# Optimization experiments

Measured on AMD Instinct MI355X. Metric: run time of the kernel, lower is better.

Reference implementation:

```python
import jax, jax.numpy as jnp
import numpy as np
from jax import lax

B, L, D, H, N, V, K = 2, 1024, 512, 8, 4, 32000, 64
HD = D // H


def layer_norm(x, g, b, eps=1e-5):
    m = jnp.mean(x, axis=-1, keepdims=True)
    v = jnp.var(x, axis=-1, keepdims=True)
    return (x - m) * lax.rsqrt(v + eps) * g + b


def setup_inputs() -> dict:
    ks = jax.random.split(jax.random.key(0), 16)
    s = 0.02
    return {
        "x_q": jax.random.normal(ks[0], (B, L, D), jnp.float32),
        "x": jax.random.randint(ks[1], (B, L), 0, V, jnp.int32),
        "E_slots": jax.random.normal(ks[2], (V, D), jnp.float32),
        "rhos": jax.random.uniform(ks[3], (N,), jnp.float32, 0.9, 0.999),
        "C_seq": jax.random.uniform(ks[4], (B, L, N), jnp.float32),
        "c_base": jax.random.uniform(ks[5], (B, K, N), jnp.float32),
        "unique_slots": jax.random.randint(ks[6], (B, K), 0, V, jnp.int32),
        "pad_mask": jnp.ones((B, K), jnp.bool_),
        "Wq": jax.random.normal(ks[7], (D, D), jnp.float32) * s,
        "Wk": jax.random.normal(ks[8], (D, D), jnp.float32) * s,
        "Wv": jax.random.normal(ks[9], (D, D), jnp.float32) * s,
        "Wo": jax.random.normal(ks[10], (D, D), jnp.float32) * s,
        "W_pe": jax.random.normal(ks[11], (N, D), jnp.float32) * s,
        "ln_kv_g": jnp.ones((D,), jnp.float32),
        "ln_kv_b": jnp.zeros((D,), jnp.float32),
        "ln_q_g": jnp.ones((D,), jnp.float32),
        "ln_q_b": jnp.zeros((D,), jnp.float32),
    }


def reference(x_q, x, E_slots, rhos, C_seq, c_base, unique_slots, pad_mask,
              Wq, Wk, Wv, Wo, W_pe, ln_kv_g, ln_kv_b, ln_q_g, ln_q_b):
    # --- projections (dropout is eval-mode identity) ---
    memory_base = layer_norm(E_slots, ln_kv_g, ln_kv_b)          # [V,D]
    E_k = (memory_base @ Wk).reshape(V, H, HD)                   # [V,H,hd]
    E_v = (memory_base @ Wv).reshape(V, H, HD)
    P_gate = (C_seq + 1.0) @ W_pe                                # [B,L,D]
    Q = layer_norm(x_q * P_gate, ln_q_g, ln_q_b) @ Wq            # [B,L,D]

    # --- initial EMA state from history ---
    safe = jnp.maximum(unique_slots, 0)                          # [B,K]
    ek0 = E_k[safe]                                              # [B,K,H,hd]
    ev0 = E_v[safe]
    outer0 = ek0[..., :, None] * ev0[..., None, :]               # [B,K,H,hd,hd]
    cb = c_base * pad_mask[..., None].astype(c_base.dtype)
    S0 = jnp.einsum('bkn,bkhij->bhnij', cb, outer0).astype(jnp.float32)  # [B,H,N,hd,hd]

    W_pe_hn = W_pe.reshape(N, H, HD).transpose(1, 0, 2)          # [H,N,hd]
    rhos_b = rhos[None, None, :, None, None]

    Qh = Q.reshape(B, L, H, HD).transpose(1, 0, 2, 3)            # [L,B,H,hd]
    toks = x.T                                                   # [L,B]

    def step(S, inp):
        q_t, tok = inp                                           # [B,H,hd], [B]
        S = S * rhos_b                                           # decay
        q_mod = q_t[:, :, None, :] * W_pe_hn[None]               # [B,H,N,hd]
        o_t = jnp.einsum('bhnd,bhnde->bhe', q_mod, S)            # sum over n, contract d
        ek_t = E_k[tok]                                          # [B,H,hd]
        ev_t = E_v[tok]
        outer = ek_t[..., :, None] * ev_t[..., None, :]          # [B,H,hd,hd]
        S = S + outer[:, :, None]                                # broadcast over N
        return S, o_t

    _, O = lax.scan(step, S0, (Qh, toks))                        # O: [L,B,H,hd]
    O = O.transpose(1, 0, 2, 3).reshape(B, L, D)
    return O @ Wo
```

## Files before the change

### kernel.cpp

```cpp
#include <hip/hip_runtime.h>
#include <stdint.h>

namespace {

constexpr int B = 2, L = 1024, D = 512, H = 8, N = 4, KSL = 64;
constexpr int CHK = 64;
constexpr int NCK = L / CHK;
constexpr int ROWS = B * L + B * KSL;

static_assert(D == 512 && N == 4, "layout assumptions");

typedef _Float16 half8 __attribute__((ext_vector_type(8)));
typedef _Float16 half4v __attribute__((ext_vector_type(4)));
typedef _Float16 half2t __attribute__((ext_vector_type(2)));
typedef float f32x4 __attribute__((ext_vector_type(4)));

__device__ __forceinline__ void gld16(_Float16* lds_dst, const _Float16* gsrc) {
  __builtin_amdgcn_global_load_lds(
      (const __attribute__((address_space(1))) unsigned int*)gsrc,
      (__attribute__((address_space(3))) unsigned int*)lds_dst, 16, 0, 0);
}

__global__ __launch_bounds__(256) void k_pre(
    const float* __restrict__ Wk, const float* __restrict__ Wv,
    const float* __restrict__ Wq, const float* __restrict__ Wo,
    _Float16* __restrict__ WTh,
    const float* __restrict__ E_slots, const int* __restrict__ x,
    const int* __restrict__ uniq, const float* __restrict__ kv_g,
    const float* __restrict__ kv_b, _Float16* __restrict__ lnEh,
    const float* __restrict__ x_q, const float* __restrict__ C_seq,
    const float* __restrict__ W_pe, const float* __restrict__ q_g,
    const float* __restrict__ q_b, _Float16* __restrict__ lnqh) {
  __shared__ _Float16 trh[64 * 66];
  __shared__ float red[8];
  int bid = blockIdx.x;
  int t = threadIdx.x;

  if (bid < 256) {
    int widx = bid >> 6, tile = bid & 63;
    int k0 = (tile >> 3) * 64, n0 = (tile & 7) * 64;
    const float* W = widx == 0 ? Wk : widx == 1 ? Wv : widx == 2 ? Wq : Wo;
#pragma unroll
    for (int i = 0; i < 16; ++i) {
      int idx = t + i * 256, r = idx >> 6, c = idx & 63;
      trh[c * 66 + r] = (_Float16)W[(size_t)(k0 + r) * 512 + n0 + c];
    }
    __syncthreads();
    _Float16* WT = WTh + (size_t)widx * 512 * 512;
#pragma unroll
    for (int i = 0; i < 8; ++i) {
      int idx = t + i * 256, rr = idx >> 5, cc = (idx & 31) * 2;
      half2t v = {trh[rr * 66 + cc], trh[rr * 66 + cc + 1]};
      *(half2t*)&WT[(size_t)(n0 + rr) * 512 + k0 + cc] = v;
    }
    return;
  }

  float vx, vy;
  const float* g;
  const float* bb;
  _Float16* dst;
  int d0 = t * 2;
  if (bid < 256 + ROWS) {
    int r = bid - 256;
    int idx;
    if (r < B * L) {
      idx = x[r];
    } else {
      int u = uniq[r - B * L];
      idx = u > 0 ? u : 0;
    }
    float2 v = *(const float2*)(E_slots + (size_t)idx * D + d0);
    vx = v.x;
    vy = v.y;
    g = kv_g; bb = kv_b;
    dst = lnEh + (size_t)r * D + d0;
  } else {
    int r = bid - 256 - ROWS;
    float c0 = C_seq[r * 4 + 0] + 1.f;
    float c1 = C_seq[r * 4 + 1] + 1.f;
    float c2 = C_seq[r * 4 + 2] + 1.f;
    float c3 = C_seq[r * 4 + 3] + 1.f;
    float p0 = c0 * W_pe[d0] + c1 * W_pe[512 + d0] + c2 * W_pe[1024 + d0] + c3 * W_pe[1536 + d0];
    float p1 = c0 * W_pe[d0 + 1] + c1 * W_pe[513 + d0] + c2 * W_pe[1025 + d0] + c3 * W_pe[1537 + d0];
    float2 xv = *(const float2*)(x_q + (size_t)r * D + d0);
    vx = xv.x * p0;
    vy = xv.y * p1;
    g = q_g; bb = q_b;
    dst = lnqh + (size_t)r * D + d0;
  }
  float s = vx + vy;
  float s2 = vx * vx + vy * vy;
#pragma unroll
  for (int o = 32; o > 0; o >>= 1) {
    s += __shfl_down(s, o);
    s2 += __shfl_down(s2, o);
  }
  if ((t & 63) == 0) {
    red[(t >> 6) * 2] = s;
    red[(t >> 6) * 2 + 1] = s2;
  }
  __syncthreads();
  float S = red[0] + red[2] + red[4] + red[6];
  float S2 = red[1] + red[3] + red[5] + red[7];
  float m = S * (1.f / D);
  float inv = rsqrtf(S2 * (1.f / D) - m * m + 1e-5f);
  half2t o2;
  o2.x = (_Float16)((vx - m) * inv * g[d0] + bb[d0]);
  o2.y = (_Float16)((vy - m) * inv * g[d0 + 1] + bb[d0 + 1]);
  *(half2t*)dst = o2;
}

__global__ __launch_bounds__(512) void k_gemm3(
    const _Float16* __restrict__ A0, const _Float16* __restrict__ Wt0, _Float16* __restrict__ C0, int M0,
    const _Float16* __restrict__ A1, const _Float16* __restrict__ Wt1, _Float16* __restrict__ C1, int M1,
    const _Float16* __restrict__ A2, const _Float16* __restrict__ Wt2, _Float16* __restrict__ C2, int M2) {
  const _Float16* A;
  const _Float16* Wt;
  _Float16* C;
  int M;
  int z = blockIdx.z;
  if (z == 0) { A = A0; Wt = Wt0; C = C0; M = M0; }
  else if (z == 1) { A = A1; Wt = Wt1; C = C1; M = M1; }
  else { A = A2; Wt = Wt2; C = C2; M = M2; }
  int m0 = blockIdx.y * 128;
  if (m0 >= M) return;
  int n0 = blockIdx.x * 128;

  __shared__ _Float16 As[2][128 * 64];
  __shared__ _Float16 Ws[2][128 * 64];

  int t = threadIdx.x;
  int lane = t & 63, w = t >> 6;
  int wr = (w >> 1) * 32, wc = (w & 1) * 64;
  int fr = lane & 15, kg = (lane >> 4) * 8;
  int kq = kg >> 3, fx = fr & 7;
  int pA = kq ^ fx, pB = (4 + kq) ^ fx;

  int srow = t >> 3;
  int sseg = ((t & 7) ^ (srow & 7)) * 8;
  int wbase = w * 512;

  const _Float16* gA = A + (size_t)(m0 + srow) * 512 + sseg;
  const _Float16* gB = Wt + (size_t)(n0 + srow) * 512 + sseg;

  f32x4 zero4 = {0.f, 0.f, 0.f, 0.f};
  f32x4 acc[2][4];
#pragma unroll
  for (int i = 0; i < 2; ++i)
#pragma unroll
    for (int j = 0; j < 4; ++j) acc[i][j] = zero4;

  gld16(&As[0][wbase], gA);
  gld16(&As[0][wbase + 4096], gA + 64 * 512);
  gld16(&Ws[0][wbase], gB);
  gld16(&Ws[0][wbase + 4096], gB + 64 * 512);
  __syncthreads();

  int buf = 0;
  for (int s8 = 0; s8 < 8; ++s8) {
    if (s8 < 7) {
      int k0 = (s8 + 1) * 64;
      gld16(&As[buf ^ 1][wbase], gA + k0);
      gld16(&As[buf ^ 1][wbase + 4096], gA + 64 * 512 + k0);
      gld16(&Ws[buf ^ 1][wbase], gB + k0);
      gld16(&Ws[buf ^ 1][wbase + 4096], gB + 64 * 512 + k0);
    }
    half8 af[2][2], bf[4][2];
#pragma unroll
    for (int mt = 0; mt < 2; ++mt) {
      int row = wr + mt * 16 + fr;
      af[mt][0] = *(const half8*)&As[buf][row * 64 + pA * 8];
      af[mt][1] = *(const half8*)&As[buf][row * 64 + pB * 8];
    }
#pragma unroll
    for (int nt = 0; nt < 4; ++nt) {
      int row = wc + nt * 16 + fr;
      bf[nt][0] = *(const half8*)&Ws[buf][row * 64 + pA * 8];
      bf[nt][1] = *(const half8*)&Ws[buf][row * 64 + pB * 8];
    }
#pragma unroll
    for (int mt = 0; mt < 2; ++mt)
#pragma unroll
      for (int nt = 0; nt < 4; ++nt) {
        acc[mt][nt] = __builtin_amdgcn_mfma_f32_16x16x32_f16(af[mt][0], bf[nt][0], acc[mt][nt], 0, 0, 0);
        acc[mt][nt] = __builtin_amdgcn_mfma_f32_16x16x32_f16(af[mt][1], bf[nt][1], acc[mt][nt], 0, 0, 0);
      }
    if (s8 < 7) __syncthreads();
    buf ^= 1;
  }
  int crow = (lane >> 4) * 4, ccol = lane & 15;
#pragma unroll
  for (int mt = 0; mt < 2; ++mt)
#pragma unroll
    for (int nt = 0; nt < 4; ++nt)
#pragma unroll
      for (int r = 0; r < 4; ++r)
        C[(size_t)(m0 + wr + mt * 16 + crow + r) * 512 + n0 + wc + nt * 16 + ccol] =
            (_Float16)acc[mt][nt][r];
}

__global__ __launch_bounds__(256) void k_gemm64(const _Float16* __restrict__ A,
                                                const _Float16* __restrict__ Wt,
                                                float* __restrict__ C) {
  int m0 = blockIdx.y * 64, n0 = blockIdx.x * 64;
  __shared__ _Float16 As[2][64 * 64];
  __shared__ _Float16 Ws[2][64 * 64];
  int t = threadIdx.x;
  int lane = t & 63, w = t >> 6;
  int wr = (w >> 1) * 32, wc = (w & 1) * 32;
  int fr = lane & 15, kg = (lane >> 4) * 8;
  int kq = kg >> 3, fx = fr & 7;
  int pA = kq ^ fx, pB = (4 + kq) ^ fx;

  int srow = t >> 3;
  int sseg = ((t & 7) ^ (srow & 7)) * 8;
  int wbase = w * 512;

  const _Float16* gA = A + (size_t)(m0 + srow) * 512 + sseg;
  const _Float16* gB = Wt + (size_t)(n0 + srow) * 512 + sseg;

  f32x4 zero4 = {0.f, 0.f, 0.f, 0.f};
  f32x4 acc[2][2];
#pragma unroll
  for (int i = 0; i < 2; ++i)
#pragma unroll
    for (int j = 0; j < 2; ++j) acc[i][j] = zero4;

  gld16(&As[0][wbase], gA);
  gld16(&As[0][wbase + 2048], gA + 32 * 512);
  gld16(&Ws[0][wbase], gB);
  gld16(&Ws[0][wbase + 2048], gB + 32 * 512);
  __syncthreads();

  int buf = 0;
  for (int s8 = 0; s8 < 8; ++s8) {
    if (s8 < 7) {
      int k0 = (s8 + 1) * 64;
      gld16(&As[buf ^ 1][wbase], gA + k0);
      gld16(&As[buf ^ 1][wbase + 2048], gA + 32 * 512 + k0);
      gld16(&Ws[buf ^ 1][wbase], gB + k0);
      gld16(&Ws[buf ^ 1][wbase + 2048], gB + 32 * 512 + k0);
    }
    half8 af[2][2], bf[2][2];
#pragma unroll
    for (int mt = 0; mt < 2; ++mt) {
      int row = wr + mt * 16 + fr;
      af[mt][0] = *(const half8*)&As[buf][row * 64 + pA * 8];
      af[mt][1] = *(const half8*)&As[buf][row * 64 + pB * 8];
    }
#pragma unroll
    for (int nt = 0; nt < 2; ++nt) {
      int row = wc + nt * 16 + fr;
      bf[nt][0] = *(const half8*)&Ws[buf][row * 64 + pA * 8];
      bf[nt][1] = *(const half8*)&Ws[buf][row * 64 + pB * 8];
    }
#pragma unroll
    for (int mt = 0; mt < 2; ++mt)
#pragma unroll
      for (int nt = 0; nt < 2; ++nt) {
        acc[mt][nt] = __builtin_amdgcn_mfma_f32_16x16x32_f16(af[mt][0], bf[nt][0], acc[mt][nt], 0, 0, 0);
        acc[mt][nt] = __builtin_amdgcn_mfma_f32_16x16x32_f16(af[mt][1], bf[nt][1], acc[mt][nt], 0, 0, 0);
      }
    if (s8 < 7) __syncthreads();
    buf ^= 1;
  }
  int crow = (lane >> 4) * 4, ccol = lane & 15;
#pragma unroll
  for (int mt = 0; mt < 2; ++mt)
#pragma unroll
    for (int nt = 0; nt < 2; ++nt)
#pragma unroll
      for (int r = 0; r < 4; ++r)
        C[(size_t)(m0 + wr + mt * 16 + crow + r) * 512 + n0 + wc + nt * 16 + ccol] =
            acc[mt][nt][r];
}

__global__ __launch_bounds__(256) void k_dct(const _Float16* __restrict__ EKh,
                                             const _Float16* __restrict__ EVh,
                                             const float* __restrict__ rhos,
                                             const float* __restrict__ c_base,
                                             _Float16* __restrict__ DCt,
                                             _Float16* __restrict__ S0t) {
  constexpr int LDH = 72;
  __shared__ _Float16 ekt[64 * LDH];
  __shared__ _Float16 evt[64 * LDH];
  __shared__ _Float16 dtab[4][64];
  int bid = blockIdx.x;
  int t = threadIdx.x;
  bool is_s0 = bid >= B * H * NCK;
  int row = t >> 2, seg = (t & 3) * 16;
  size_t grow;
  if (!is_s0) {
    int c = bid % NCK, h = (bid / NCK) % H, b = bid / (NCK * H);
    grow = (size_t)(b * L + c * CHK + row) * 512 + h * 64 + seg;
    int nn = t >> 6, uu = t & 63;
    dtab[nn][uu] = (_Float16)exp2f((float)(CHK - uu) * log2f(rhos[nn]));
  } else {
    int bh = bid - B * H * NCK;
    int h = bh % H, b = bh / H;
    grow = (size_t)(B * L + b * KSL + row) * 512 + h * 64 + seg;
    int nn = t >> 6, uu = t & 63;
    dtab[nn][uu] = (_Float16)c_base[(b * KSL + uu) * N + nn];
  }
  half8 e0 = *(const half8*)(EKh + grow);
  half8 e1 = *(const half8*)(EKh + grow + 8);
  half8 v0 = *(const half8*)(EVh + grow);
  half8 v1 = *(const half8*)(EVh + grow + 8);
#pragma unroll
  for (int i = 0; i < 8; ++i) {
    ekt[(seg + i) * LDH + row] = e0[i];
    ekt[(seg + 8 + i) * LDH + row] = e1[i];
    evt[(seg + i) * LDH + row] = v0[i];
    evt[(seg + 8 + i) * LDH + row] = v1[i];
  }
  __syncthreads();

  int lane = t & 63, w = t >> 6;
  int wr = (w >> 1) * 32, wc = (w & 1) * 32;
  int fr = lane & 15, kg = (lane >> 4) * 8;
  int crow = (lane >> 4) * 4, ccol = lane & 15;

  half8 ef[2][2], bf[2][2];
#pragma unroll
  for (int mt = 0; mt < 2; ++mt)
#pragma unroll
    for (int ks = 0; ks < 2; ++ks)
      ef[mt][ks] = *(const half8*)&evt[(wr + mt * 16 + fr) * LDH + ks * 32 + kg];
#pragma unroll
  for (int nt = 0; nt < 2; ++nt)
#pragma unroll
    for (int ks = 0; ks < 2; ++ks)
      bf[nt][ks] = *(const half8*)&ekt[(wc + nt * 16 + fr) * LDH + ks * 32 + kg];

  f32x4 zero4 = {0.f, 0.f, 0.f, 0.f};
#pragma unroll
  for (int n = 0; n < 4; ++n) {
    half8 dec0 = *(const half8*)&dtab[n][kg];
    half8 dec1 = *(const half8*)&dtab[n][32 + kg];
    half8 af0a = ef[0][0] * dec0, af0b = ef[0][1] * dec1;
    half8 af1a = ef[1][0] * dec0, af1b = ef[1][1] * dec1;
    f32x4 acc[2][2];
#pragma unroll
    for (int i = 0; i < 2; ++i)
#pragma unroll
      for (int j = 0; j < 2; ++j) acc[i][j] = zero4;
#pragma unroll
    for (int nt = 0; nt < 2; ++nt) {
      acc[0][nt] = __builtin_amdgcn_mfma_f32_16x16x32_f16(af0a, bf[nt][0], acc[0][nt], 0, 0, 0);
      acc[0][nt] = __builtin_amdgcn_mfma_f32_16x16x32_f16(af0b, bf[nt][1], acc[0][nt], 0, 0, 0);
      acc[1][nt] = __builtin_amdgcn_mfma_f32_16x16x32_f16(af1a, bf[nt][0], acc[1][nt], 0, 0, 0);
      acc[1][nt] = __builtin_amdgcn_mfma_f32_16x16x32_f16(af1b, bf[nt][1], acc[1][nt], 0, 0, 0);
    }
    _Float16* dp = is_s0 ? S0t + ((size_t)(bid - B * H * NCK) * N + n) * 4096
                         : DCt + ((size_t)bid * N + n) * 4096;
#pragma unroll
    for (int mt = 0; mt < 2; ++mt)
#pragma unroll
      for (int nt = 0; nt < 2; ++nt)
#pragma unroll
        for (int r = 0; r < 4; ++r)
          dp[(wr + mt * 16 + crow + r) * 64 + wc + nt * 16 + ccol] = (_Float16)acc[mt][nt][r];
  }
}

__global__ void k_gscan(const _Float16* __restrict__ S0t, const _Float16* __restrict__ DCt,
                        const float* __restrict__ rhos, _Float16* __restrict__ GT) {
  int bhn = blockIdx.x >> 2, sl = blockIdx.x & 3;
  int n = bhn % N, bh = bhn / N;
  float rho = rhos[n];
  float rhoC = exp2f(64.f * log2f(rho));
  int off = sl * 1024 + threadIdx.x * 4;
  half4v dc[NCK];
#pragma unroll
  for (int c = 0; c < NCK; ++c)
    dc[c] = *(const half4v*)(DCt + ((size_t)(bh * NCK + c) * N + n) * 4096 + off);
  half4v s0 = *(const half4v*)(S0t + (size_t)bhn * 4096 + off);
  float gv[4];
#pragma unroll
  for (int i = 0; i < 4; ++i) gv[i] = rho * (float)s0[i];
  _Float16* gp = GT + (size_t)bhn * NCK * 4096 + off;
#pragma unroll
  for (int cc = 0; cc < NCK; ++cc) {
    half4v o;
#pragma unroll
    for (int i = 0; i < 4; ++i) o[i] = (_Float16)gv[i];
    *(half4v*)(gp + (size_t)cc * 4096) = o;
#pragma unroll
    for (int i = 0; i < 4; ++i) gv[i] = rhoC * gv[i] + (float)dc[cc][i];
  }
}

__global__ __launch_bounds__(256) void k_chunk(
    const _Float16* __restrict__ Qh, const _Float16* __restrict__ EKh,
    const _Float16* __restrict__ EVh, const _Float16* __restrict__ GT,
    const float* __restrict__ W_pe, const float* __restrict__ rhos,
    _Float16* __restrict__ OAh) {
  int bid = blockIdx.x;
  int c = bid % NCK, h = (bid / NCK) % H, b = bid / (NCK * H);
  constexpr int LDH = 72;
  __shared__ _Float16 qs[64 * LDH];
  __shared__ _Float16 eks[64 * LDH];
  __shared__ _Float16 evt[64 * LDH];
  __shared__ _Float16 gts[4][64 * LDH];
  __shared__ _Float16 wsm[64 * LDH];
  __shared__ _Float16 wpeh[4][64];
  __shared__ float rup[4][64];
  __shared__ float rvi[4][64];
  int t = threadIdx.x;
  {
    int row = t >> 2, seg = (t & 3) * 16;
    size_t grow = (size_t)(b * L + c * CHK + row) * 512 + h * 64 + seg;
    half8 q0 = *(const half8*)(Qh + grow);
    half8 q1 = *(const half8*)(Qh + grow + 8);
    half8 k0 = *(const half8*)(EKh + grow);
    half8 k1 = *(const half8*)(EKh + grow + 8);
    half8 v0 = *(const half8*)(EVh + grow);
    half8 v1 = *(const half8*)(EVh + grow + 8);
    *(half8*)&qs[row * LDH + seg] = q0;
    *(half8*)&qs[row * LDH + seg + 8] = q1;
    *(half8*)&eks[row * LDH + seg] = k0;
    *(half8*)&eks[row * LDH + seg + 8] = k1;
#pragma unroll
    for (int i = 0; i < 8; ++i) {
      evt[(seg + i) * LDH + row] = v0[i];
      evt[(seg + 8 + i) * LDH + row] = v1[i];
    }
#pragma unroll
    for (int n = 0; n < 4; ++n) {
      const _Float16* gpp = GT + (((size_t)(b * H + h) * N + n) * NCK + c) * 4096 + row * 64 + seg;
      *(half8*)&gts[n][row * LDH + seg] = *(const half8*)gpp;
      *(half8*)&gts[n][row * LDH + seg + 8] = *(const half8*)(gpp + 8);
    }
    int nn = t >> 6, dd = t & 63;
    float l2r = log2f(rhos[nn]);
    wpeh[nn][dd] = (_Float16)W_pe[nn * 512 + h * 64 + dd];
    rup[nn][dd] = exp2f((float)dd * l2r);
    rvi[nn][dd] = exp2f(-(float)dd * l2r);
  }
  __syncthreads();

  int lane = t & 63, w = t >> 6;
  int u0 = w * 16;
  int fr = lane & 15, kg = (lane >> 4) * 8;
  int crow = (lane >> 4) * 4, ccol = lane & 15;

  half8 qf0 = *(const half8*)&qs[(u0 + fr) * LDH + kg];
  half8 qf1 = *(const half8*)&qs[(u0 + fr) * LDH + 32 + kg];

  f32x4 zero4 = {0.f, 0.f, 0.f, 0.f};
  f32x4 oa[4], wacc[4];
#pragma unroll
  for (int i = 0; i < 4; ++i) { oa[i] = zero4; wacc[i] = zero4; }

#pragma unroll
  for (int n = 0; n < 4; ++n) {
    half8 am0 = qf0 * (*(const half8*)&wpeh[n][kg]);
    half8 am1 = qf1 * (*(const half8*)&wpeh[n][32 + kg]);
    float ru[4];
#pragma unroll
    for (int r = 0; r < 4; ++r) ru[r] = rup[n][u0 + crow + r];
#pragma unroll
    for (int et = 0; et < 4; ++et) {
      f32x4 ta = zero4;
      ta = __builtin_amdgcn_mfma_f32_16x16x32_f16(
          am0, *(const half8*)&gts[n][(et * 16 + fr) * LDH + kg], ta, 0, 0, 0);
      ta = __builtin_amdgcn_mfma_f32_16x16x32_f16(
          am1, *(const half8*)&gts[n][(et * 16 + fr) * LDH + 32 + kg], ta, 0, 0, 0);
#pragma unroll
      for (int r = 0; r < 4; ++r) oa[et][r] += ru[r] * ta[r];
    }
#pragma unroll
    for (int vt = 0; vt < 4; ++vt) {
      f32x4 sa = zero4;
      sa = __builtin_amdgcn_mfma_f32_16x16x32_f16(
          am0, *(const half8*)&eks[(vt * 16 + fr) * LDH + kg], sa, 0, 0, 0);
      sa = __builtin_amdgcn_mfma_f32_16x16x32_f16(
          am1, *(const half8*)&eks[(vt * 16 + fr) * LDH + 32 + kg], sa, 0, 0, 0);
      int v = vt * 16 + ccol;
      float rv = rvi[n][v];
#pragma unroll
      for (int r = 0; r < 4; ++r) {
        int u = u0 + crow + r;
        float coef = (v < u) ? ru[r] * rv : 0.f;
        wacc[vt][r] += coef * sa[r];
      }
    }
  }
#pragma unroll
  for (int vt = 0; vt < 4; ++vt)
#pragma unroll
    for (int r = 0; r < 4; ++r)
      wsm[(u0 + crow + r) * LDH + vt * 16 + ccol] = (_Float16)wacc[vt][r];
  half8 wf0 = *(const half8*)&wsm[(u0 + fr) * LDH + kg];
  half8 wf1 = *(const half8*)&wsm[(u0 + fr) * LDH + 32 + kg];
#pragma unroll
  for (int et = 0; et < 4; ++et) {
    oa[et] = __builtin_amdgcn_mfma_f32_16x16x32_f16(
        wf0, *(const half8*)&evt[(et * 16 + fr) * LDH + kg], oa[et], 0, 0, 0);
    oa[et] = __builtin_amdgcn_mfma_f32_16x16x32_f16(
        wf1, *(const half8*)&evt[(et * 16 + fr) * LDH + 32 + kg], oa[et], 0, 0, 0);
  }
#pragma unroll
  for (int et = 0; et < 4; ++et)
#pragma unroll
    for (int r = 0; r < 4; ++r)
      OAh[(size_t)(b * L + c * CHK + u0 + crow + r) * 512 + h * 64 + et * 16 + ccol] =
          (_Float16)oa[et][r];
}

}

extern "C" void kernel_launch(void* const* d_in, const int* in_sizes, int n_in,
                              void* d_out, int out_size, void* d_ws, size_t ws_size,
                              hipStream_t stream) {
  const float* x_q = (const float*)d_in[0];
  const int* x = (const int*)d_in[1];
  const float* E_slots = (const float*)d_in[2];
  const float* rhos = (const float*)d_in[3];
  const float* C_seq = (const float*)d_in[4];
  const float* c_base = (const float*)d_in[5];
  const int* uniq = (const int*)d_in[6];
  const float* Wq = (const float*)d_in[8];
  const float* Wk = (const float*)d_in[9];
  const float* Wv = (const float*)d_in[10];
  const float* Wo = (const float*)d_in[11];
  const float* W_pe = (const float*)d_in[12];
  const float* ln_kv_g = (const float*)d_in[13];
  const float* ln_kv_b = (const float*)d_in[14];
  const float* ln_q_g = (const float*)d_in[15];
  const float* ln_q_b = (const float*)d_in[16];
  float* out = (float*)d_out;

  _Float16* hb = (_Float16*)d_ws;
  _Float16* lnEh = hb;
  _Float16* lnqh = lnEh + 1114112;
  _Float16* WTh = lnqh + 1048576;
  _Float16* EKh = WTh + 1048576;
  _Float16* EVh = EKh + 1114112;
  _Float16* Qh = EVh + 1114112;
  _Float16* DCt = Qh + 1048576;
  _Float16* S0t = DCt + 4194304;
  _Float16* GT = S0t + 262144;
  _Float16* OAh = GT + 4194304;

  const _Float16* WTk = WTh;
  const _Float16* WTv = WTh + 262144;
  const _Float16* WTq = WTh + 524288;
  const _Float16* WTo = WTh + 786432;

  k_pre<<<256 + ROWS + B * L, 256, 0, stream>>>(
      Wk, Wv, Wq, Wo, WTh, E_slots, x, uniq, ln_kv_g, ln_kv_b, lnEh,
      x_q, C_seq, W_pe, ln_q_g, ln_q_b, lnqh);
  k_gemm3<<<dim3(4, 17, 3), 512, 0, stream>>>(lnEh, WTk, EKh, ROWS,
                                              lnEh, WTv, EVh, ROWS,
                                              lnqh, WTq, Qh, B * L);
  k_dct<<<B * H * NCK + B * H, 256, 0, stream>>>(EKh, EVh, rhos, c_base, DCt, S0t);
  k_gscan<<<B * H * N * 4, 256, 0, stream>>>(S0t, DCt, rhos, GT);
  k_chunk<<<B * H * NCK, 256, 0, stream>>>(Qh, EKh, EVh, GT, W_pe, rhos, OAh);
  k_gemm64<<<dim3(8, 32), 256, 0, stream>>>(OAh, WTo, out);
}
```

Before: 44.84 us.

## Fuse inter-chunk state scan into chunk kernel, recomputing prefix per block

Removes the separate k_gscan kernel and its GT buffer. Each k_chunk block now rebuilds its own chunk-start state by walking the decayed prefix sum of DCt entries up to its chunk index. This saves one kernel launch and the write and read of the GT array. In exchange it adds redundant work: late chunks read up to 15 DCt tiles per n, so global reads grow and blocks become unbalanced.

New measurement: 57.17 us. +27.5%, slower.

```diff
diff --git a/kernel.cpp b/kernel.cpp
--- a/kernel.cpp
+++ b/kernel.cpp
@@ -364,40 +364,14 @@
   }
 }
 
-__global__ void k_gscan(const _Float16* __restrict__ S0t, const _Float16* __restrict__ DCt,
-                        const float* __restrict__ rhos, _Float16* __restrict__ GT) {
-  int bhn = blockIdx.x >> 2, sl = blockIdx.x & 3;
-  int n = bhn % N, bh = bhn / N;
-  float rho = rhos[n];
-  float rhoC = exp2f(64.f * log2f(rho));
-  int off = sl * 1024 + threadIdx.x * 4;
-  half4v dc[NCK];
-#pragma unroll
-  for (int c = 0; c < NCK; ++c)
-    dc[c] = *(const half4v*)(DCt + ((size_t)(bh * NCK + c) * N + n) * 4096 + off);
-  half4v s0 = *(const half4v*)(S0t + (size_t)bhn * 4096 + off);
-  float gv[4];
-#pragma unroll
-  for (int i = 0; i < 4; ++i) gv[i] = rho * (float)s0[i];
-  _Float16* gp = GT + (size_t)bhn * NCK * 4096 + off;
-#pragma unroll
-  for (int cc = 0; cc < NCK; ++cc) {
-    half4v o;
-#pragma unroll
-    for (int i = 0; i < 4; ++i) o[i] = (_Float16)gv[i];
-    *(half4v*)(gp + (size_t)cc * 4096) = o;
-#pragma unroll
-    for (int i = 0; i < 4; ++i) gv[i] = rhoC * gv[i] + (float)dc[cc][i];
-  }
-}
-
 __global__ __launch_bounds__(256) void k_chunk(
     const _Float16* __restrict__ Qh, const _Float16* __restrict__ EKh,
-    const _Float16* __restrict__ EVh, const _Float16* __restrict__ GT,
-    const float* __restrict__ W_pe, const float* __restrict__ rhos,
-    _Float16* __restrict__ OAh) {
+    const _Float16* __restrict__ EVh, const _Float16* __restrict__ S0t,
+    const _Float16* __restrict__ DCt, const float* __restrict__ W_pe,
+    const float* __restrict__ rhos, _Float16* __restrict__ OAh) {
   int bid = blockIdx.x;
   int c = bid % NCK, h = (bid / NCK) % H, b = bid / (NCK * H);
+  int bh = b * H + h;
   constexpr int LDH = 72;
   __shared__ _Float16 qs[64 * LDH];
   __shared__ _Float16 eks[64 * LDH];
@@ -426,11 +400,38 @@
       evt[(seg + i) * LDH + row] = v0[i];
       evt[(seg + 8 + i) * LDH + row] = v1[i];
     }
+    int tileoff = row * 64 + seg;
 #pragma unroll
     for (int n = 0; n < 4; ++n) {
-      const _Float16* gpp = GT + (((size_t)(b * H + h) * N + n) * NCK + c) * 4096 + row * 64 + seg;
-      *(half8*)&gts[n][row * LDH + seg] = *(const half8*)gpp;
-      *(half8*)&gts[n][row * LDH + seg + 8] = *(const half8*)(gpp + 8);
+      float rho = rhos[n];
+      float rhoC = exp2f(64.f * log2f(rho));
+      const _Float16* s0p = S0t + ((size_t)bh * N + n) * 4096 + tileoff;
+      half8 sa = *(const half8*)s0p;
+      half8 sb = *(const half8*)(s0p + 8);
+      float ga[8], gb[8];
+#pragma unroll
+      for (int i = 0; i < 8; ++i) {
+        ga[i] = rho * (float)sa[i];
+        gb[i] = rho * (float)sb[i];
+      }
+      for (int j = 0; j < c; ++j) {
+        const _Float16* dp = DCt + (((size_t)bh * NCK + j) * N + n) * 4096 + tileoff;
+        half8 da = *(const half8*)dp;
+        half8 db = *(const half8*)(dp + 8);
+#pragma unroll
+        for (int i = 0; i < 8; ++i) {
+          ga[i] = rhoC * ga[i] + (float)da[i];
+          gb[i] = rhoC * gb[i] + (float)db[i];
+        }
+      }
+      half8 oga, ogb;
+#pragma unroll
+      for (int i = 0; i < 8; ++i) {
+        oga[i] = (_Float16)ga[i];
+        ogb[i] = (_Float16)gb[i];
+      }
+      *(half8*)&gts[n][row * LDH + seg] = oga;
+      *(half8*)&gts[n][row * LDH + seg + 8] = ogb;
     }
     int nn = t >> 6, dd = t & 63;
     float l2r = log2f(rhos[nn]);
@@ -541,8 +542,7 @@
   _Float16* Qh = EVh + 1114112;
   _Float16* DCt = Qh + 1048576;
   _Float16* S0t = DCt + 4194304;
-  _Float16* GT = S0t + 262144;
-  _Float16* OAh = GT + 4194304;
+  _Float16* OAh = S0t + 262144;
 
   const _Float16* WTk = WTh;
   const _Float16* WTv = WTh + 262144;
@@ -556,7 +556,6 @@
                                               lnEh, WTv, EVh, ROWS,
                                               lnqh, WTq, Qh, B * L);
   k_dct<<<B * H * NCK + B * H, 256, 0, stream>>>(EKh, EVh, rhos, c_base, DCt, S0t);
-  k_gscan<<<B * H * N * 4, 256, 0, stream>>>(S0t, DCt, rhos, GT);
-  k_chunk<<<B * H * NCK, 256, 0, stream>>>(Qh, EKh, EVh, GT, W_pe, rhos, OAh);
+  k_chunk<<<B * H * NCK, 256, 0, stream>>>(Qh, EKh, EVh, S0t, DCt, W_pe, rhos, OAh);
   k_gemm64<<<dim3(8, 32), 256, 0, stream>>>(OAh, WTo, out);
 }
```
